# Kernel tuning notes

Measured on AMD Instinct MI355X. Metric: run time of the kernel, lower is better.

The kernel has to match this reference:

```python
import jax, jax.numpy as jnp
import numpy as np

B, N, K = 8192, 2048, 4  # batch, nodes, neighbors (original: 45, 168, 4)


def _collect_and_transfer(x, adj):
    # x: (B, N), adj: (N, K) int indices of neighbors.
    # Original builds, per node i, a (B, K) block of gathered neighbor values,
    # stacks to (N, B, K), then raw-reshapes (view) to (B, 1, K, N).
    g = jnp.transpose(x[:, adj], (1, 0, 2))   # (N, B, K)
    return g.reshape(x.shape[0], 1, K, adj.shape[0])  # memory reinterpretation, as in .view


def reference(x, label, adj, conv_w, conv_b, lin_w, lin_b):
    a = jnp.concatenate([_collect_and_transfer(x, adj),
                         _collect_and_transfer(label, adj)], axis=1)  # (B, 2, K, N)
    # Conv2d(2 -> 1, kernel=(1,4), stride=(1,4)): (B, 1, K, N//4)
    y = jax.lax.conv_general_dilated(
        a, conv_w, window_strides=(1, 4), padding='VALID',
        dimension_numbers=('NCHW', 'OIHW', 'NCHW'))
    y = jax.nn.relu(y + conv_b[None, :, None, None])
    y = y.reshape(B, N)              # K * (N//4) == N
    return y @ lin_w.T + lin_b       # Linear(N, N)


def setup_inputs() -> dict:
    key = jax.random.key(0)
    k1, k2, k3, k4, k5 = jax.random.split(key, 5)
    return {
        'x': jax.random.normal(k1, (B, N), dtype=jnp.float32),
        'label': jax.random.normal(k2, (B, N), dtype=jnp.float32),
        'adj': jax.random.randint(k3, (N, K), 0, N, dtype=jnp.int32),
        'conv_w': jax.random.normal(k4, (1, 2, 1, 4), dtype=jnp.float32) * 0.1,
        'conv_b': jnp.zeros((1,), dtype=jnp.float32),
        'lin_w': jax.random.normal(k5, (N, N), dtype=jnp.float32) * 0.02,
        'lin_b': jnp.zeros((N,), dtype=jnp.float32),
    }
```

## Files before the change

kernel.cpp:

```cpp
#include <hip/hip_runtime.h>

typedef __bf16 bf16;
typedef bf16 bf16x8 __attribute__((ext_vector_type(8)));
typedef bf16 bf16x4 __attribute__((ext_vector_type(4)));
typedef float f32x4 __attribute__((ext_vector_type(4)));
typedef unsigned short ushort;
typedef ushort ushort4v __attribute__((ext_vector_type(4)));

#define BB 8192
#define NN 2048

__device__ __forceinline__ void async16(const void* g, void* l) {
    __builtin_amdgcn_global_load_lds(
        (__attribute__((address_space(1))) void*)(void*)g,
        (__attribute__((address_space(3))) void*)l,
        16, 0, 0);
}

__global__ __launch_bounds__(256) void conv_gather(
    const float* __restrict__ x, const float* __restrict__ label,
    const int* __restrict__ adj, const float* __restrict__ cw,
    const float* __restrict__ cb, bf16* __restrict__ V) {
    __shared__ float sx[2][NN];
    __shared__ float sl[2][NN];
    const int bb0 = blockIdx.x * 2;
    const int t   = threadIdx.x;

#pragma unroll
    for (int rr = 0; rr < 2; ++rr) {
        const float4* xr = (const float4*)(x     + (size_t)(bb0 + rr) * NN);
        const float4* lr = (const float4*)(label + (size_t)(bb0 + rr) * NN);
#pragma unroll
        for (int q = 0; q < 2; ++q) {
            int i = q * 256 + t;
            ((float4*)sx[rr])[i] = xr[i];
            ((float4*)sl[rr])[i] = lr[i];
        }
    }
    const float w0 = cw[0], w1 = cw[1], w2 = cw[2], w3 = cw[3];
    const float w4 = cw[4], w5 = cw[5], w6 = cw[6], w7 = cw[7];
    const float bias = cb[0];

    const int4* adj4 = (const int4*)adj;
    int4 a[8];
#pragma unroll
    for (int j = 0; j < 8; ++j) a[j] = adj4[t * 8 + j];

    __syncthreads();

#pragma unroll
    for (int rr = 0; rr < 2; ++rr) {
        const float* px = sx[rr];
        const float* pl = sl[rr];
        bf16 o[8];
#pragma unroll
        for (int j = 0; j < 8; ++j) {
            int4 aa = a[j];
            float v = bias
                    + w0 * px[aa.x] + w1 * px[aa.y] + w2 * px[aa.z] + w3 * px[aa.w]
                    + w4 * pl[aa.x] + w5 * pl[aa.y] + w6 * pl[aa.z] + w7 * pl[aa.w];
            o[j] = (bf16)fmaxf(v, 0.0f);
        }
        *(bf16x8*)(V + (size_t)(bb0 + rr) * NN + t * 8) = *(const bf16x8*)o;
    }
}

__global__ __launch_bounds__(256) void cvtw(const float* __restrict__ W,
                                            bf16* __restrict__ Wb) {
    size_t i = (size_t)blockIdx.x * 256 + threadIdx.x;
    float4 v0 = ((const float4*)W)[i * 2 + 0];
    float4 v1 = ((const float4*)W)[i * 2 + 1];
    bf16x8 o;
    o[0] = (bf16)v0.x; o[1] = (bf16)v0.y; o[2] = (bf16)v0.z; o[3] = (bf16)v0.w;
    o[4] = (bf16)v1.x; o[5] = (bf16)v1.y; o[6] = (bf16)v1.z; o[7] = (bf16)v1.w;
    ((bf16x8*)Wb)[i] = o;
}

__global__ __launch_bounds__(256) void transp(const ushort* __restrict__ V,
                                              ushort* __restrict__ Y) {
    __shared__ ushort tile[64][68];
    const int g0 = blockIdx.x * 64;
    const int p0 = blockIdx.y * 64;
    const int c  = threadIdx.x & 15;
    const int r4 = threadIdx.x >> 4;

#pragma unroll
    for (int pass = 0; pass < 4; ++pass) {
        int r = pass * 16 + r4;
        ushort4v v = *(const ushort4v*)(V + (size_t)(p0 + r) * NN + g0 + c * 4);
        *(ushort4v*)&tile[r][c * 4] = v;
    }
    __syncthreads();
#pragma unroll
    for (int pass = 0; pass < 4; ++pass) {
        int r = pass * 16 + r4;
        ushort4v o;
        o.x = tile[c * 4 + 0][r];
        o.y = tile[c * 4 + 1][r];
        o.z = tile[c * 4 + 2][r];
        o.w = tile[c * 4 + 3][r];
        *(ushort4v*)(Y + (size_t)(g0 + r) * BB + p0 + c * 4) = o;
    }
}

__global__ __launch_bounds__(256) void gemm_bt(
    const bf16* __restrict__ A, const bf16* __restrict__ W,
    const float* __restrict__ bias, float* __restrict__ out) {
    __shared__ __attribute__((aligned(16))) bf16 sA[128 * 32];
    __shared__ __attribute__((aligned(16))) bf16 sB[128 * 32];

    const int t    = threadIdx.x;
    const int lane = t & 63;
    const int wv   = t >> 6;
    const int wm   = wv & 1;
    const int wn   = wv >> 1;
    const int m0   = blockIdx.x * 128;
    const int n0   = blockIdx.y * 128;

    f32x4 acc[4][4] = {};

    const int r  = t >> 2;
    const int c8 = (t & 3) * 8;
    const bf16* gA0 = A + (size_t)(m0 + r)      * 2048 + c8;
    const bf16* gA1 = A + (size_t)(m0 + r + 64) * 2048 + c8;
    const bf16* gB0 = W + (size_t)(n0 + r)      * 2048 + c8;
    const bf16* gB1 = W + (size_t)(n0 + r + 64) * 2048 + c8;
    bf16* lA0 = sA + (wv * 16)      * 32;
    bf16* lA1 = sA + (64 + wv * 16) * 32;
    bf16* lB0 = sB + (wv * 16)      * 32;
    bf16* lB1 = sB + (64 + wv * 16) * 32;

    const int quad = lane >> 4;
    const int l16  = lane & 15;
    const bf16* fA = sA + (wm * 64 + l16) * 32 + quad * 8;
    const bf16* fB = sB + (wn * 64 + l16) * 32 + quad * 8;

    for (int k0 = 0; k0 < 2048; k0 += 32) {
        async16(gA0 + k0, lA0);
        async16(gA1 + k0, lA1);
        async16(gB0 + k0, lB0);
        async16(gB1 + k0, lB1);
        __syncthreads();

        bf16x8 af[4], bfr[4];
#pragma unroll
        for (int i = 0; i < 4; ++i) af[i]  = *(const bf16x8*)(fA + i * 16 * 32);
#pragma unroll
        for (int j = 0; j < 4; ++j) bfr[j] = *(const bf16x8*)(fB + j * 16 * 32);
#pragma unroll
        for (int i = 0; i < 4; ++i)
#pragma unroll
            for (int j = 0; j < 4; ++j)
                acc[i][j] = __builtin_amdgcn_mfma_f32_16x16x32_bf16(
                    af[i], bfr[j], acc[i][j], 0, 0, 0);
        __syncthreads();
    }

#pragma unroll
    for (int j = 0; j < 4; ++j) {
        int col = n0 + wn * 64 + j * 16 + l16;
        float bcol = bias[col];
#pragma unroll
        for (int i = 0; i < 4; ++i) {
            int rowb = m0 + wm * 64 + i * 16 + quad * 4;
#pragma unroll
            for (int rr = 0; rr < 4; ++rr) {
                out[(size_t)(rowb + rr) * 2048 + col] = acc[i][j][rr] + bcol;
            }
        }
    }
}

extern "C" void kernel_launch(void* const* d_in, const int* in_sizes, int n_in,
                              void* d_out, int out_size, void* d_ws, size_t ws_size,
                              hipStream_t stream) {
    (void)in_sizes; (void)n_in; (void)out_size; (void)ws_size;
    const float* x     = (const float*)d_in[0];
    const float* label = (const float*)d_in[1];
    const int*   adj   = (const int*)d_in[2];
    const float* cw    = (const float*)d_in[3];
    const float* cb    = (const float*)d_in[4];
    const float* lw    = (const float*)d_in[5];
    const float* lb    = (const float*)d_in[6];
    float* out = (float*)d_out;

    bf16* V  = (bf16*)d_out;
    bf16* Y2 = (bf16*)d_ws;
    bf16* Wb = (bf16*)((char*)d_ws + (size_t)2048 * 8192 * 2);

    conv_gather<<<BB / 2, 256, 0, stream>>>(x, label, adj, cw, cb, V);
    cvtw<<<2048, 256, 0, stream>>>(lw, Wb);
    transp<<<dim3(32, 128), 256, 0, stream>>>((const ushort*)V, (ushort*)Y2);
    gemm_bt<<<dim3(64, 16), 256, 0, stream>>>(Y2, Wb, lb, out);
}
```

Baseline: 313.9 us.

## Interleave conv inputs in LDS, merge transpose with weight cast, deepen GEMM k-step

The conv/gather kernel now stores x and label for both batch rows interleaved as float4 in shared memory, so each neighbor index needs one LDS read instead of four. The weight bf16 conversion and the transpose are merged into one launch, removing a kernel launch. The GEMM loads two 32-wide k-slices per barrier pair, halving the number of syncs per k, at the cost of double the LDS footprint.

```diff
diff --git a/kernel.cpp b/kernel.cpp
--- a/kernel.cpp
+++ b/kernel.cpp
@@ -2,7 +2,6 @@
 
 typedef __bf16 bf16;
 typedef bf16 bf16x8 __attribute__((ext_vector_type(8)));
-typedef bf16 bf16x4 __attribute__((ext_vector_type(4)));
 typedef float f32x4 __attribute__((ext_vector_type(4)));
 typedef unsigned short ushort;
 typedef ushort ushort4v __attribute__((ext_vector_type(4)));
@@ -21,21 +20,22 @@
     const float* __restrict__ x, const float* __restrict__ label,
     const int* __restrict__ adj, const float* __restrict__ cw,
     const float* __restrict__ cb, bf16* __restrict__ V) {
-    __shared__ float sx[2][NN];
-    __shared__ float sl[2][NN];
+    __shared__ float4 sxl[NN];
     const int bb0 = blockIdx.x * 2;
     const int t   = threadIdx.x;
 
-#pragma unroll
-    for (int rr = 0; rr < 2; ++rr) {
-        const float4* xr = (const float4*)(x     + (size_t)(bb0 + rr) * NN);
-        const float4* lr = (const float4*)(label + (size_t)(bb0 + rr) * NN);
-#pragma unroll
-        for (int q = 0; q < 2; ++q) {
-            int i = q * 256 + t;
-            ((float4*)sx[rr])[i] = xr[i];
-            ((float4*)sl[rr])[i] = lr[i];
-        }
+    const float4* x0 = (const float4*)(x     + (size_t)bb0 * NN);
+    const float4* x1 = (const float4*)(x     + (size_t)(bb0 + 1) * NN);
+    const float4* l0 = (const float4*)(label + (size_t)bb0 * NN);
+    const float4* l1 = (const float4*)(label + (size_t)(bb0 + 1) * NN);
+#pragma unroll
+    for (int q = 0; q < 2; ++q) {
+        int i = q * 256 + t;
+        float4 a = x0[i], b = l0[i], c = x1[i], d = l1[i];
+        sxl[i*4+0] = make_float4(a.x, b.x, c.x, d.x);
+        sxl[i*4+1] = make_float4(a.y, b.y, c.y, d.y);
+        sxl[i*4+2] = make_float4(a.z, b.z, c.z, d.z);
+        sxl[i*4+3] = make_float4(a.w, b.w, c.w, d.w);
     }
     const float w0 = cw[0], w1 = cw[1], w2 = cw[2], w3 = cw[3];
     const float w4 = cw[4], w5 = cw[5], w6 = cw[6], w7 = cw[7];
@@ -48,39 +48,44 @@
 
     __syncthreads();
 
-#pragma unroll
-    for (int rr = 0; rr < 2; ++rr) {
-        const float* px = sx[rr];
-        const float* pl = sl[rr];
-        bf16 o[8];
-#pragma unroll
-        for (int j = 0; j < 8; ++j) {
-            int4 aa = a[j];
-            float v = bias
-                    + w0 * px[aa.x] + w1 * px[aa.y] + w2 * px[aa.z] + w3 * px[aa.w]
-                    + w4 * pl[aa.x] + w5 * pl[aa.y] + w6 * pl[aa.z] + w7 * pl[aa.w];
-            o[j] = (bf16)fmaxf(v, 0.0f);
-        }
-        *(bf16x8*)(V + (size_t)(bb0 + rr) * NN + t * 8) = *(const bf16x8*)o;
-    }
-}
-
-__global__ __launch_bounds__(256) void cvtw(const float* __restrict__ W,
-                                            bf16* __restrict__ Wb) {
-    size_t i = (size_t)blockIdx.x * 256 + threadIdx.x;
-    float4 v0 = ((const float4*)W)[i * 2 + 0];
-    float4 v1 = ((const float4*)W)[i * 2 + 1];
-    bf16x8 o;
-    o[0] = (bf16)v0.x; o[1] = (bf16)v0.y; o[2] = (bf16)v0.z; o[3] = (bf16)v0.w;
-    o[4] = (bf16)v1.x; o[5] = (bf16)v1.y; o[6] = (bf16)v1.z; o[7] = (bf16)v1.w;
-    ((bf16x8*)Wb)[i] = o;
-}
-
-__global__ __launch_bounds__(256) void transp(const ushort* __restrict__ V,
-                                              ushort* __restrict__ Y) {
+    bf16 o0[8], o1[8];
+#pragma unroll
+    for (int j = 0; j < 8; ++j) {
+        int4 aa = a[j];
+        float4 p0 = sxl[aa.x];
+        float4 p1 = sxl[aa.y];
+        float4 p2 = sxl[aa.z];
+        float4 p3 = sxl[aa.w];
+        float v0 = bias
+                 + w0 * p0.x + w1 * p1.x + w2 * p2.x + w3 * p3.x
+                 + w4 * p0.y + w5 * p1.y + w6 * p2.y + w7 * p3.y;
+        float v1 = bias
+                 + w0 * p0.z + w1 * p1.z + w2 * p2.z + w3 * p3.z
+                 + w4 * p0.w + w5 * p1.w + w6 * p2.w + w7 * p3.w;
+        o0[j] = (bf16)fmaxf(v0, 0.0f);
+        o1[j] = (bf16)fmaxf(v1, 0.0f);
+    }
+    *(bf16x8*)(V + (size_t)bb0 * NN + t * 8)       = *(const bf16x8*)o0;
+    *(bf16x8*)(V + (size_t)(bb0 + 1) * NN + t * 8) = *(const bf16x8*)o1;
+}
+
+__global__ __launch_bounds__(256) void transp_cvtw(
+    const ushort* __restrict__ V, ushort* __restrict__ Y,
+    const float* __restrict__ W, bf16* __restrict__ Wb) {
+    const int b = blockIdx.x;
+    if (b >= 4096) {
+        size_t i = (size_t)(b - 4096) * 256 + threadIdx.x;
+        float4 v0 = ((const float4*)W)[i * 2 + 0];
+        float4 v1 = ((const float4*)W)[i * 2 + 1];
+        bf16x8 o;
+        o[0] = (bf16)v0.x; o[1] = (bf16)v0.y; o[2] = (bf16)v0.z; o[3] = (bf16)v0.w;
+        o[4] = (bf16)v1.x; o[5] = (bf16)v1.y; o[6] = (bf16)v1.z; o[7] = (bf16)v1.w;
+        ((bf16x8*)Wb)[i] = o;
+        return;
+    }
     __shared__ ushort tile[64][68];
-    const int g0 = blockIdx.x * 64;
-    const int p0 = blockIdx.y * 64;
+    const int g0 = (b & 31) * 64;
+    const int p0 = (b >> 5) * 64;
     const int c  = threadIdx.x & 15;
     const int r4 = threadIdx.x >> 4;
 
@@ -106,8 +111,8 @@
 __global__ __launch_bounds__(256) void gemm_bt(
     const bf16* __restrict__ A, const bf16* __restrict__ W,
     const float* __restrict__ bias, float* __restrict__ out) {
-    __shared__ __attribute__((aligned(16))) bf16 sA[128 * 32];
-    __shared__ __attribute__((aligned(16))) bf16 sB[128 * 32];
+    __shared__ __attribute__((aligned(16))) bf16 sA[2][128 * 32];
+    __shared__ __attribute__((aligned(16))) bf16 sB[2][128 * 32];
 
     const int t    = threadIdx.x;
     const int lane = t & 63;
@@ -125,34 +130,46 @@
     const bf16* gA1 = A + (size_t)(m0 + r + 64) * 2048 + c8;
     const bf16* gB0 = W + (size_t)(n0 + r)      * 2048 + c8;
     const bf16* gB1 = W + (size_t)(n0 + r + 64) * 2048 + c8;
-    bf16* lA0 = sA + (wv * 16)      * 32;
-    bf16* lA1 = sA + (64 + wv * 16) * 32;
-    bf16* lB0 = sB + (wv * 16)      * 32;
-    bf16* lB1 = sB + (64 + wv * 16) * 32;
+    bf16* lA0[2], *lA1[2], *lB0[2], *lB1[2];
+#pragma unroll
+    for (int s = 0; s < 2; ++s) {
+        lA0[s] = sA[s] + (wv * 16)      * 32;
+        lA1[s] = sA[s] + (64 + wv * 16) * 32;
+        lB0[s] = sB[s] + (wv * 16)      * 32;
+        lB1[s] = sB[s] + (64 + wv * 16) * 32;
+    }
 
     const int quad = lane >> 4;
     const int l16  = lane & 15;
-    const bf16* fA = sA + (wm * 64 + l16) * 32 + quad * 8;
-    const bf16* fB = sB + (wn * 64 + l16) * 32 + quad * 8;
-
-    for (int k0 = 0; k0 < 2048; k0 += 32) {
-        async16(gA0 + k0, lA0);
-        async16(gA1 + k0, lA1);
-        async16(gB0 + k0, lB0);
-        async16(gB1 + k0, lB1);
+    const int foff = (wm * 64 + l16) * 32 + quad * 8;
+    const int goff = (wn * 64 + l16) * 32 + quad * 8;
+
+    for (int k0 = 0; k0 < 2048; k0 += 64) {
+#pragma unroll
+        for (int s = 0; s < 2; ++s) {
+            async16(gA0 + k0 + s * 32, lA0[s]);
+            async16(gA1 + k0 + s * 32, lA1[s]);
+            async16(gB0 + k0 + s * 32, lB0[s]);
+            async16(gB1 + k0 + s * 32, lB1[s]);
+        }
         __syncthreads();
 
-        bf16x8 af[4], bfr[4];
-#pragma unroll
-        for (int i = 0; i < 4; ++i) af[i]  = *(const bf16x8*)(fA + i * 16 * 32);
-#pragma unroll
-        for (int j = 0; j < 4; ++j) bfr[j] = *(const bf16x8*)(fB + j * 16 * 32);
-#pragma unroll
-        for (int i = 0; i < 4; ++i)
-#pragma unroll
-            for (int j = 0; j < 4; ++j)
-                acc[i][j] = __builtin_amdgcn_mfma_f32_16x16x32_bf16(
-                    af[i], bfr[j], acc[i][j], 0, 0, 0);
+#pragma unroll
+        for (int s = 0; s < 2; ++s) {
+            const bf16* fA = sA[s] + foff;
+            const bf16* fB = sB[s] + goff;
+            bf16x8 af[4], bfr[4];
+#pragma unroll
+            for (int i = 0; i < 4; ++i) af[i]  = *(const bf16x8*)(fA + i * 16 * 32);
+#pragma unroll
+            for (int j = 0; j < 4; ++j) bfr[j] = *(const bf16x8*)(fB + j * 16 * 32);
+#pragma unroll
+            for (int i = 0; i < 4; ++i)
+#pragma unroll
+                for (int j = 0; j < 4; ++j)
+                    acc[i][j] = __builtin_amdgcn_mfma_f32_16x16x32_bf16(
+                        af[i], bfr[j], acc[i][j], 0, 0, 0);
+        }
         __syncthreads();
     }
 
@@ -189,7 +206,7 @@
     bf16* Wb = (bf16*)((char*)d_ws + (size_t)2048 * 8192 * 2);
 
     conv_gather<<<BB / 2, 256, 0, stream>>>(x, label, adj, cw, cb, V);
-    cvtw<<<2048, 256, 0, stream>>>(lw, Wb);
-    transp<<<dim3(32, 128), 256, 0, stream>>>((const ushort*)V, (ushort*)Y2);
+    transp_cvtw<<<6144, 256, 0, stream>>>((const ushort*)V, (ushort*)Y2,
+                                          lw, Wb);
     gemm_bt<<<dim3(64, 16), 256, 0, stream>>>(Y2, Wb, lb, out);
 }
```

After: 281.7 us. 10.3% less time.
